# Kernel optimization log

Measured on AMD Instinct MI355X. Metric: run time of the kernel, lower is better.

Reference implementation:

```python
import jax, jax.numpy as jnp
import numpy as np

D = 256       # vec_dim
HEADS = 8     # head_num
PS = 4        # patch_size
WS = 7        # window_size (in patches)
P = WS * WS   # tokens per window


def _relative_index():
    # replicates the torch meshgrid / relative coord logic (indexing='ij')
    coords = np.stack(np.meshgrid(np.arange(WS), np.arange(WS), indexing='ij'))  # [2,WS,WS]
    cf = coords.reshape(2, -1)                                                   # [2,P]
    rc = (cf[:, :, None] - cf[:, None, :]).transpose(1, 2, 0)                    # [P,P,2]
    rc[:, :, 0] += WS - 1
    rc[:, :, 1] += WS - 1
    rc[:, :, 1] *= 2 * WS - 1
    return rc.sum(-1)  # [P,P] ints in [0,(2WS-1)^2)


def _shift_mask(ch, cw):
    # standard swin shift mask built on the patch grid (ch, cw)
    fm = np.zeros((ch, cw))
    idx = (slice(0, -WS), slice(-WS, -(WS // 2)), slice(-(WS // 2), None))
    cnt = 0
    for y in idx:
        for x in idx:
            fm[y, x] = cnt
            cnt += 1
    nh, nw = ch // WS, cw // WS
    fm = fm.reshape(nh, WS, nw, WS).transpose(0, 2, 1, 3).reshape(nh * nw, P)
    m = fm[:, None, :] - fm[:, :, None]
    return np.where(m != 0, -100.0, 0.0).astype(np.float32)


def setup_inputs() -> dict:
    key = jax.random.key(0)
    ks = jax.random.split(key, 10)
    N, PN = 8, 3136
    s = 0.02
    return {
        'inputs': jax.random.normal(ks[0], (N, D, PN), jnp.float32),
        'Wk': jax.random.normal(ks[1], (HEADS * D, D), jnp.float32) * s,
        'bk': jax.random.normal(ks[2], (HEADS * D,), jnp.float32) * s,
        'Wq': jax.random.normal(ks[3], (HEADS * D, D), jnp.float32) * s,
        'bq': jax.random.normal(ks[4], (HEADS * D,), jnp.float32) * s,
        'Wv': jax.random.normal(ks[5], (HEADS * D, D), jnp.float32) * s,
        'bv': jax.random.normal(ks[6], (HEADS * D,), jnp.float32) * s,
        'Wo': jax.random.normal(ks[7], (D, HEADS * D), jnp.float32) * s,
        'bo': jax.random.normal(ks[8], (D,), jnp.float32) * s,
        'rel_code': jax.random.normal(ks[9], ((2 * WS - 1) ** 2, HEADS), jnp.float32) * 0.02,
        'h': 224,
        'w': 224,
    }


def _forward(inputs, Wk, bk, Wq, bq, Wv, bv, Wo, bo, rel_code, h, w):
    ch, cw = h // PS, w // PS            # patch grid
    N, _, PN = inputs.shape
    C = D // (PS * PS)
    nh, nw = ch // WS, cw // WS
    WIN = nh * nw

    # patches2features -> pixel-space roll by WS//2 -> features2patches
    x = inputs.reshape(N, C, PS, PS, ch, cw)
    x = x.transpose(0, 1, 4, 2, 5, 3).reshape(N, C, ch * PS, cw * PS)
    x = jnp.roll(x, (WS // 2, WS // 2), axis=(-2, -1))
    x = x.reshape(N, C, ch, PS, cw, PS).transpose(0, 2, 4, 1, 3, 5).reshape(N, PN, D)
    x = x.transpose(0, 2, 1)  # [N,D,PN]

    def proj(W, b):
        e = jnp.einsum('od,ndp->nop', W, x) + b[None, :, None]  # [N,HEADS*D,PN]
        e = e.reshape(N, HEADS, D, ch, cw)
        # window partition: n h d (nh w1)(nw w2) -> n h (nh nw) d (w1 w2)
        e = e.reshape(N, HEADS, D, nh, WS, nw, WS)
        return e.transpose(0, 1, 3, 5, 2, 4, 6).reshape(N, HEADS, WIN, D, P)

    k = proj(Wk, bk)
    q = proj(Wq, bq)
    v = proj(Wv, bv)

    # attn[p,q] = k_p . q_q  (softmax over keys p, axis=3)
    attn = jnp.einsum('nhgdp,nhgdq->nhgpq', k, q) / (D ** 0.5)
    mask = jnp.asarray(_shift_mask(ch, cw))
    attn = attn + mask[None, None]
    rel_idx = _relative_index().ravel()
    rel = rel_code[rel_idx].reshape(P, P, HEADS).transpose(2, 0, 1)  # [H,P,P]
    attn = attn + rel[None, :, None]
    wmap = jax.nn.softmax(attn, axis=3)

    out = jnp.einsum('nhgdp,nhgpq->nhgdq', v, wmap)
    # window merge back to [N,H,D,PN]
    out = out.reshape(N, HEADS, nh, nw, D, WS, WS)
    out = out.transpose(0, 1, 4, 2, 5, 3, 6).reshape(N, HEADS * D, PN)
    return jnp.einsum('od,ndp->nop', Wo, out) + bo[None, :, None]  # [N,D,PN]


def reference(inputs, Wk, bk, Wq, bq, Wv, bv, Wo, bo, rel_code, h, w):
    return _forward(inputs, Wk, bk, Wq, bq, Wv, bv, Wo, bo, rel_code, h, w)
```

## Files before the change

### kernel.cpp

```cpp
#include <hip/hip_runtime.h>
#include <hip/hip_bf16.h>


#define NBATCH 8
#define TROWS  3200
#define FSTR   264

typedef unsigned short ushort_t;
typedef __attribute__((ext_vector_type(8))) short bf16x8;
typedef __attribute__((ext_vector_type(8))) unsigned short u16x8;
typedef __attribute__((ext_vector_type(4))) float f32x4;

__device__ __forceinline__ float b2f(ushort_t u) {
  union { unsigned int i; float f; } v; v.i = ((unsigned int)u) << 16; return v.f;
}
__device__ __forceinline__ ushort_t f2b(float f) {
  union { float f; unsigned int u; } v; v.f = f;
  unsigned int u = v.u;
  return (ushort_t)((u + 0x7FFFu + ((u >> 16) & 1u)) >> 16);
}
__device__ __forceinline__ int regof(int y) { return (y < 49) ? 0 : ((y < 53) ? 1 : 2); }
__device__ __forceinline__ int div7(int t) { return (t * 37) >> 8; }
__device__ __forceinline__ int tmap(int p, int gi, int gj) {
  int wi = div7(p); return (gi * 7 + wi) * 56 + gj * 7 + (p - wi * 7);
}
__device__ __forceinline__ ushort4 pack4(f32x4 a) {
  ushort4 u; u.x = f2b(a[0]); u.y = f2b(a[1]); u.z = f2b(a[2]); u.w = f2b(a[3]);
  return u;
}

__global__ void k_prep(const float* __restrict__ Wk, const float* __restrict__ Wq,
                       const float* __restrict__ Wo, const float* __restrict__ Wv,
                       const float* __restrict__ bk, const float* __restrict__ bq,
                       const float* __restrict__ bv, const float* __restrict__ bo,
                       const float* __restrict__ relc,
                       ushort_t* __restrict__ Aext, ushort_t* __restrict__ Wov3,
                       float* __restrict__ cvec, float* __restrict__ relL2) {
  __shared__ float red[8];
  int blk = blockIdx.x, t = threadIdx.x;
  if (blk < 512) {
    int h = blk >> 6, b0 = (blk & 63) << 2, a = t;
    const float* wkh = Wk + h * 65536;
    const float* wqh = Wq + h * 65536;
    float a0 = 0.f, a1 = 0.f, a2 = 0.f, a3 = 0.f;
    for (int dd = 0; dd < 256; ++dd) {
      float wk = wkh[dd * 256 + a];
      float4 w4 = *(const float4*)(wqh + dd * 256 + b0);
      a0 += wk * w4.x; a1 += wk * w4.y; a2 += wk * w4.z; a3 += wk * w4.w;
    }
    ushort4 u; u.x = f2b(a0); u.y = f2b(a1); u.z = f2b(a2); u.w = f2b(a3);
    *(ushort4*)(Aext + (h * 256 + a) * 256 + b0) = u;
  } else if (blk < 1024) {
    int bb = blk - 512;
    int h = bb >> 6, o0 = (bb & 63) << 2, d = t;
    float a0 = 0.f, a1 = 0.f, a2 = 0.f, a3 = 0.f;
    for (int dd = 0; dd < 256; ++dd) {
      float wv = Wv[(h * 256 + dd) * 256 + d];
      a0 += Wo[(o0 + 0) * 2048 + h * 256 + dd] * wv;
      a1 += Wo[(o0 + 1) * 2048 + h * 256 + dd] * wv;
      a2 += Wo[(o0 + 2) * 2048 + h * 256 + dd] * wv;
      a3 += Wo[(o0 + 3) * 2048 + h * 256 + dd] * wv;
    }
    Wov3[(o0 + 0) * 2048 + h * 256 + d] = f2b(a0);
    Wov3[(o0 + 1) * 2048 + h * 256 + d] = f2b(a1);
    Wov3[(o0 + 2) * 2048 + h * 256 + d] = f2b(a2);
    Wov3[(o0 + 3) * 2048 + h * 256 + d] = f2b(a3);
  } else if (blk < 1032) {
    int h = blk - 1024;
    float s1 = 0.f, s2 = 0.f;
    for (int dd = 0; dd < 256; ++dd) {
      s1 += bk[h * 256 + dd] * Wq[(h * 256 + dd) * 256 + t];
      s2 += bq[h * 256 + dd] * Wk[(h * 256 + dd) * 256 + t];
    }
    Aext[(2048 + h) * 256 + t] = f2b(s1);
    Aext[(2056 + h) * 256 + t] = f2b(s2);
  } else if (blk == 1032) {
    for (int i = t; i < 112 * 256 / 8; i += 256)
      *(u16x8*)(Aext + 2064 * 256 + i * 8) = (u16x8){0,0,0,0,0,0,0,0};
  } else if (blk < 1289) {
    int o = blk - 1033;
    const float* wob = Wo + o * 2048;
    float acc = 0.f;
#pragma unroll
    for (int j = 0; j < 8; ++j) acc += wob[j * 256 + t] * bv[j * 256 + t];
#pragma unroll
    for (int s = 1; s < 64; s <<= 1) acc += __shfl_xor(acc, s);
    if ((t & 63) == 0) red[t >> 6] = acc;
    __syncthreads();
    if (t == 0) cvec[o] = bo[o] + red[0] + red[1] + red[2] + red[3];
  } else {
    if (t < 8) {
      float c = 0.f;
      for (int dd = 0; dd < 256; ++dd) c += bk[t * 256 + dd] * bq[t * 256 + dd];
      red[t] = c * 0.0625f;
    }
    __syncthreads();
    for (int i = t; i < 8 * 169; i += 256) {
      int h = i / 169, idx = i - h * 169;
      relL2[i] = relc[idx * 8 + h] + red[h];
    }
  }
}

__global__ void k_conv(const float* __restrict__ X, ushort_t* __restrict__ Xroll) {
  const int n = blockIdx.x / 57, y = blockIdx.x % 57;
  ushort_t* xr = Xroll + (size_t)n * TROWS * 256;
  const int d = threadIdx.x;
  if (y == 56) {
    for (int i = d; i < 64 * 256 / 8; i += 256)
      *(u16x8*)(xr + 3136 * 256 + i * 8) = (u16x8){0,0,0,0,0,0,0,0};
    return;
  }
  const int c = d >> 4, p1 = (d >> 2) & 3, p2 = d & 3;
  const int sp = c * 16 + (((p1 + 1) & 3) << 2) + ((p2 + 1) & 3);
  const int ty = (p1 == 3) ? y : ((y == 0) ? 55 : y - 1);
  const float* rowp = X + (size_t)n * 256 * 3136 + sp * 3136 + ty * 56;
  ushort_t* orow = xr + y * 56 * 256 + d;
  for (int x = 0; x < 56; ++x) {
    int tx = (p2 == 3) ? x : ((x == 0) ? 55 : x - 1);
    orow[x * 256] = f2b(rowp[tx]);
  }
}

__global__ __launch_bounds__(512, 1) void k_fused(
    const ushort_t* __restrict__ Xroll, const ushort_t* __restrict__ Aext,
    const ushort_t* __restrict__ Wov3, const float* __restrict__ cvec,
    const float* __restrict__ relL2, float* __restrict__ out) {
  __shared__ ushort_t Xp[64 * FSTR];
  __shared__ ushort_t Msm[64 * FSTR];
  __shared__ ushort_t Tsm[64 * FSTR];
  __shared__ ushort_t StB[64 * 72];
  __shared__ float aqsL[8 * 64];
  __shared__ float bpsL[8 * 64];
  __shared__ float relLh[8 * 169];
  __shared__ float mPart[2][64];
  __shared__ float sPart[2][64];

  const int tid = threadIdx.x;
  const int wave = tid >> 6, lane = tid & 63;
  const int quad = lane >> 4, l16 = lane & 15;
  const int n = blockIdx.x & 7, g = blockIdx.x >> 3;
  const int gi = g >> 3, gj = g & 7;
  const ushort_t* Xn = Xroll + (size_t)n * TROWS * 256;
  float* on = out + (size_t)n * 256 * 3136;

  {
    const int p = tid & 63, cg = tid >> 6;
    if (p < 49) {
      int t = tmap(p, gi, gj);
#pragma unroll
      for (int i = 0; i < 4; ++i)
        *(u16x8*)(&Xp[p * FSTR + (cg * 4 + i) * 8]) =
            *(const u16x8*)(Xn + t * 256 + (cg * 4 + i) * 8);
    } else {
#pragma unroll
      for (int i = 0; i < 4; ++i)
        *(u16x8*)(&Xp[p * FSTR + (cg * 4 + i) * 8]) = (u16x8){0,0,0,0,0,0,0,0};
    }
  }
  for (int i = tid; i < 8 * 169; i += 512) relLh[i] = relL2[i];
  __syncthreads();

  const int wp = wave >> 2;
  const int wq = wave & 3;

  bf16x8 xb[8][2];
#pragma unroll
  for (int kk = 0; kk < 8; ++kk)
#pragma unroll
    for (int j = 0; j < 2; ++j)
      xb[kk][j] = *(const bf16x8*)(&Xp[((wp * 2 + j) * 16 + l16) * FSTR + kk * 32 + quad * 8]);

  bf16x8 xfr[2][2];
#pragma unroll
  for (int dt = 0; dt < 2; ++dt) {
    const int d = (wave * 2 + dt) * 16 + l16;
#pragma unroll
    for (int kk = 0; kk < 2; ++kk)
#pragma unroll
      for (int j = 0; j < 8; ++j)
        xfr[dt][kk][j] = (short)Xp[(kk * 32 + quad * 8 + j) * FSTR + d];
  }

  auto m_step = [&](int h) {
    f32x4 macc[2][4];
#pragma unroll
    for (int i = 0; i < 2; ++i)
#pragma unroll
      for (int t = 0; t < 4; ++t) macc[i][t] = (f32x4){0.f, 0.f, 0.f, 0.f};
    const ushort_t* Ah =
        Aext + (size_t)(h * 256 + wave * 32 + l16) * 256 + quad * 8;
#pragma unroll
    for (int kk = 0; kk < 8; ++kk) {
      bf16x8 ga[2];
#pragma unroll
      for (int i = 0; i < 2; ++i)
        ga[i] = *(const bf16x8*)(Ah + i * 16 * 256 + kk * 32);
#pragma unroll
      for (int t = 0; t < 4; ++t) {
        bf16x8 bx_ = *(const bf16x8*)(&Xp[(t * 16 + l16) * FSTR + kk * 32 + quad * 8]);
#pragma unroll
        for (int i = 0; i < 2; ++i)
          macc[i][t] = __builtin_amdgcn_mfma_f32_16x16x32_bf16(ga[i], bx_, macc[i][t], 0, 0, 0);
      }
    }
#pragma unroll
    for (int i = 0; i < 2; ++i)
#pragma unroll
      for (int t = 0; t < 4; ++t)
        *(ushort4*)(&Msm[(t * 16 + l16) * FSTR + wave * 32 + i * 16 + quad * 4]) =
            pack4(macc[i][t]);
  };

  m_step(0);
  if (wave == 0) {
    f32x4 eacc[4];
#pragma unroll
    for (int t = 0; t < 4; ++t) eacc[t] = (f32x4){0.f, 0.f, 0.f, 0.f};
    const ushort_t* Ae = Aext + (size_t)(2048 + l16) * 256 + quad * 8;
#pragma unroll
    for (int kk = 0; kk < 8; ++kk) {
      bf16x8 ea = *(const bf16x8*)(Ae + kk * 32);
#pragma unroll
      for (int t = 0; t < 4; ++t) {
        bf16x8 bx_ = *(const bf16x8*)(&Xp[(t * 16 + l16) * FSTR + kk * 32 + quad * 8]);
        eacc[t] = __builtin_amdgcn_mfma_f32_16x16x32_bf16(ea, bx_, eacc[t], 0, 0, 0);
      }
    }
#pragma unroll
    for (int t = 0; t < 4; ++t) {
      const int tok = t * 16 + l16;
#pragma unroll
      for (int r = 0; r < 4; ++r) {
        const int e = quad * 4 + r;
        if (e < 8) aqsL[e * 64 + tok] = eacc[t][r];
        else       bpsL[(e - 8) * 64 + tok] = eacc[t][r];
      }
    }
  }
  __syncthreads();

  const int q = wq * 16 + l16;
  const int qq = (q < 49) ? q : 48;
  const int yq = div7(qq), xq = qq - yq * 7;
  const int fq = regof(gi * 7 + yq) * 3 + regof(gj * 7 + xq);

  f32x4 oacc[2][4];
#pragma unroll
  for (int i = 0; i < 2; ++i)
#pragma unroll
    for (int j = 0; j < 4; ++j) oacc[i][j] = (f32x4){0.f, 0.f, 0.f, 0.f};

  for (int h = 0; h < 8; ++h) {
    f32x4 sa0[2], sa1[2];
    sa0[0] = (f32x4){0.f,0.f,0.f,0.f}; sa0[1] = (f32x4){0.f,0.f,0.f,0.f};
    sa1[0] = (f32x4){0.f,0.f,0.f,0.f}; sa1[1] = (f32x4){0.f,0.f,0.f,0.f};
#pragma unroll
    for (int kk = 0; kk < 8; kk += 2) {
      bf16x8 bfm0 = *(const bf16x8*)(&Msm[q * FSTR + kk * 32 + quad * 8]);
      bf16x8 bfm1 = *(const bf16x8*)(&Msm[q * FSTR + (kk + 1) * 32 + quad * 8]);
#pragma unroll
      for (int j = 0; j < 2; ++j) {
        sa0[j] = __builtin_amdgcn_mfma_f32_16x16x32_bf16(xb[kk][j], bfm0, sa0[j], 0, 0, 0);
        sa1[j] = __builtin_amdgcn_mfma_f32_16x16x32_bf16(xb[kk + 1][j], bfm1, sa1[j], 0, 0, 0);
      }
    }
    float v[8], ew[8];
    const float aqv = aqsL[h * 64 + q];
    const float* rel_h = &relLh[h * 169];
    float mw = -1e30f;
#pragma unroll
    for (int j = 0; j < 2; ++j)
#pragma unroll
      for (int r = 0; r < 4; ++r) {
        const int p = (wp * 2 + j) * 16 + quad * 4 + r;
        float val = -1e30f;
        if (p < 49) {
          const int yp = div7(p), xp = p - yp * 7;
          const int fp = regof(gi * 7 + yp) * 3 + regof(gj * 7 + xp);
          val = (sa0[j][r] + sa1[j][r] + aqv + bpsL[h * 64 + p]) * 0.0625f +
                rel_h[(yp - yq + 6) + 13 * (xp - xq + 6)];
          if (fp != fq) val -= 100.f;
        }
        v[j * 4 + r] = val;
        mw = fmaxf(mw, val);
      }
    mw = fmaxf(mw, __shfl_xor(mw, 16));
    mw = fmaxf(mw, __shfl_xor(mw, 32));
    float sw = 0.f;
#pragma unroll
    for (int i2 = 0; i2 < 8; ++i2) { ew[i2] = __expf(v[i2] - mw); sw += ew[i2]; }
    sw += __shfl_xor(sw, 16);
    sw += __shfl_xor(sw, 32);
    if (lane < 16) { mPart[wp][wq * 16 + lane] = mw; sPart[wp][wq * 16 + lane] = sw; }
    __syncthreads();
    {
      const float m0 = mPart[0][q], m1 = mPart[1][q];
      const float s0 = sPart[0][q], s1 = sPart[1][q];
      const float mg = fmaxf(m0, m1);
      const float tot = s0 * __expf(m0 - mg) + s1 * __expf(m1 - mg);
      const float scale = __expf(mw - mg) / tot;
#pragma unroll
      for (int j = 0; j < 2; ++j) {
        ushort4 u;
        u.x = f2b(ew[j * 4 + 0] * scale); u.y = f2b(ew[j * 4 + 1] * scale);
        u.z = f2b(ew[j * 4 + 2] * scale); u.w = f2b(ew[j * 4 + 3] * scale);
        *(ushort4*)(&StB[q * 72 + (wp * 2 + j) * 16 + quad * 4]) = u;
      }
    }
    if (h < 7) m_step(h + 1);
    __syncthreads();
    bf16x8 wfr[2][8];
#pragma unroll
    for (int i = 0; i < 2; ++i)
#pragma unroll
      for (int kk = 0; kk < 8; ++kk)
        wfr[i][kk] = *(const bf16x8*)(Wov3 +
            (size_t)(wave * 32 + i * 16 + l16) * 2048 + h * 256 + kk * 32 + quad * 8);
#pragma unroll
    for (int qt = 0; qt < 4; ++qt) {
      f32x4 tacc[2];
      tacc[0] = (f32x4){0.f, 0.f, 0.f, 0.f};
      tacc[1] = (f32x4){0.f, 0.f, 0.f, 0.f};
#pragma unroll
      for (int kk = 0; kk < 2; ++kk) {
        bf16x8 bfw = *(const bf16x8*)(&StB[(qt * 16 + l16) * 72 + kk * 32 + quad * 8]);
#pragma unroll
        for (int dt = 0; dt < 2; ++dt)
          tacc[dt] = __builtin_amdgcn_mfma_f32_16x16x32_bf16(xfr[dt][kk], bfw, tacc[dt], 0, 0, 0);
      }
#pragma unroll
      for (int dt = 0; dt < 2; ++dt)
        *(ushort4*)(&Tsm[(qt * 16 + l16) * FSTR + (wave * 2 + dt) * 16 + quad * 4]) =
            pack4(tacc[dt]);
    }
    __syncthreads();
#pragma unroll
    for (int kk = 0; kk < 8; ++kk) {
#pragma unroll
      for (int qt = 0; qt < 4; ++qt) {
        bf16x8 bfo = *(const bf16x8*)(&Tsm[(qt * 16 + l16) * FSTR + kk * 32 + quad * 8]);
#pragma unroll
        for (int i = 0; i < 2; ++i)
          oacc[i][qt] = __builtin_amdgcn_mfma_f32_16x16x32_bf16(wfr[i][kk], bfo, oacc[i][qt], 0, 0, 0);
      }
    }
  }
#pragma unroll
  for (int i = 0; i < 2; ++i) {
    const int ob = wave * 32 + i * 16 + quad * 4;
    const float4 cv = *(const float4*)(cvec + ob);
#pragma unroll
    for (int qt = 0; qt < 4; ++qt) {
      const int q2 = qt * 16 + l16;
      if (q2 < 49) {
        const int t2 = tmap(q2, gi, gj);
        on[(size_t)(ob + 0) * 3136 + t2] = oacc[i][qt][0] + cv.x;
        on[(size_t)(ob + 1) * 3136 + t2] = oacc[i][qt][1] + cv.y;
        on[(size_t)(ob + 2) * 3136 + t2] = oacc[i][qt][2] + cv.z;
        on[(size_t)(ob + 3) * 3136 + t2] = oacc[i][qt][3] + cv.w;
      }
    }
  }
}

extern "C" void kernel_launch(void* const* d_in, const int* in_sizes, int n_in,
                              void* d_out, int out_size, void* d_ws, size_t ws_size,
                              hipStream_t stream) {
  (void)in_sizes; (void)n_in; (void)out_size; (void)ws_size;
  const float* X  = (const float*)d_in[0];
  const float* Wk = (const float*)d_in[1];
  const float* bk = (const float*)d_in[2];
  const float* Wq = (const float*)d_in[3];
  const float* bq = (const float*)d_in[4];
  const float* Wv = (const float*)d_in[5];
  const float* bv = (const float*)d_in[6];
  const float* Wo = (const float*)d_in[7];
  const float* bo = (const float*)d_in[8];
  const float* rc = (const float*)d_in[9];

  ushort_t* Xroll = (ushort_t*)d_ws;
  ushort_t* Aext  = Xroll + (size_t)8 * TROWS * 256;
  ushort_t* Wov3  = Aext + 2176 * 256;
  float* fbase = (float*)(Wov3 + 256 * 2048);
  float* cvec  = fbase;
  float* relL2 = fbase + 256;
  float* out = (float*)d_out;

  k_prep <<<dim3(1290), dim3(256), 0, stream>>>(Wk, Wq, Wo, Wv, bk, bq, bv, bo, rc,
                                                Aext, Wov3, cvec, relL2);
  k_conv <<<dim3(8 * 57), dim3(256), 0, stream>>>(X, Xroll);
  k_fused<<<dim3(512), dim3(512), 0, stream>>>(Xroll, Aext, Wov3, cvec, relL2, out);
}
```

Before: 297.4 us.

## Double fused kernel block to 1024 threads and split per-wave work

The fused attention kernel now runs 16 waves per block instead of 8. Each wave's share of the M projection, score, softmax, T and output GEMMs is halved by re-partitioning tokens and output rows, and softmax partials are now combined across four wave groups. The Wo fragment loads are split into two halves to cut register pressure. The conv/roll kernel also loads each input row with vectorized float4 reads into registers instead of doing scalar gathered loads. The change aims for more latency hiding and fewer registers per wave, at the cost of more synchronization participants and a wider cross-wave softmax reduction.

```diff
diff --git a/kernel.cpp b/kernel.cpp
--- a/kernel.cpp
+++ b/kernel.cpp
@@ -116,13 +116,22 @@
   const int ty = (p1 == 3) ? y : ((y == 0) ? 55 : y - 1);
   const float* rowp = X + (size_t)n * 256 * 3136 + sp * 3136 + ty * 56;
   ushort_t* orow = xr + y * 56 * 256 + d;
+  float row[56];
+#pragma unroll
+  for (int i = 0; i < 14; ++i) {
+    const float4 t4 = ((const float4*)rowp)[i];
+    row[i * 4 + 0] = t4.x; row[i * 4 + 1] = t4.y;
+    row[i * 4 + 2] = t4.z; row[i * 4 + 3] = t4.w;
+  }
+  const bool nr = (p2 == 3);
+#pragma unroll
   for (int x = 0; x < 56; ++x) {
-    int tx = (p2 == 3) ? x : ((x == 0) ? 55 : x - 1);
-    orow[x * 256] = f2b(rowp[tx]);
-  }
-}
-
-__global__ __launch_bounds__(512, 1) void k_fused(
+    const float a = (x == 0) ? row[55] : row[x - 1];
+    orow[x * 256] = f2b(nr ? row[x] : a);
+  }
+}
+
+__global__ __launch_bounds__(1024, 4) void k_fused(
     const ushort_t* __restrict__ Xroll, const ushort_t* __restrict__ Aext,
     const ushort_t* __restrict__ Wov3, const float* __restrict__ cvec,
     const float* __restrict__ relL2, float* __restrict__ out) {
@@ -133,8 +142,8 @@
   __shared__ float aqsL[8 * 64];
   __shared__ float bpsL[8 * 64];
   __shared__ float relLh[8 * 169];
-  __shared__ float mPart[2][64];
-  __shared__ float sPart[2][64];
+  __shared__ float mPart[4][64];
+  __shared__ float sPart[4][64];
 
   const int tid = threadIdx.x;
   const int wave = tid >> 6, lane = tid & 63;
@@ -149,47 +158,47 @@
     if (p < 49) {
       int t = tmap(p, gi, gj);
 #pragma unroll
-      for (int i = 0; i < 4; ++i)
-        *(u16x8*)(&Xp[p * FSTR + (cg * 4 + i) * 8]) =
-            *(const u16x8*)(Xn + t * 256 + (cg * 4 + i) * 8);
+      for (int i = 0; i < 2; ++i)
+        *(u16x8*)(&Xp[p * FSTR + (cg * 2 + i) * 8]) =
+            *(const u16x8*)(Xn + t * 256 + (cg * 2 + i) * 8);
     } else {
 #pragma unroll
-      for (int i = 0; i < 4; ++i)
-        *(u16x8*)(&Xp[p * FSTR + (cg * 4 + i) * 8]) = (u16x8){0,0,0,0,0,0,0,0};
-    }
-  }
-  for (int i = tid; i < 8 * 169; i += 512) relLh[i] = relL2[i];
+      for (int i = 0; i < 2; ++i)
+        *(u16x8*)(&Xp[p * FSTR + (cg * 2 + i) * 8]) = (u16x8){0,0,0,0,0,0,0,0};
+    }
+  }
+  for (int i = tid; i < 8 * 169; i += 1024) relLh[i] = relL2[i];
   __syncthreads();
 
-  const int wp = wave >> 2;
-  const int wq = wave & 3;
-
-  bf16x8 xb[8][2];
+  const int wq  = wave & 3,  wpt = wave >> 2;
+  const int wb  = wave & 7,  th  = wave >> 3;
+  const int qp  = wave & 1,  dg  = wave >> 1;
+  const int wo  = wave & 7,  wq2 = wave >> 3;
+
+  bf16x8 xb[8];
 #pragma unroll
   for (int kk = 0; kk < 8; ++kk)
-#pragma unroll
-    for (int j = 0; j < 2; ++j)
-      xb[kk][j] = *(const bf16x8*)(&Xp[((wp * 2 + j) * 16 + l16) * FSTR + kk * 32 + quad * 8]);
+    xb[kk] = *(const bf16x8*)(&Xp[(wpt * 16 + l16) * FSTR + kk * 32 + quad * 8]);
 
   bf16x8 xfr[2][2];
 #pragma unroll
   for (int dt = 0; dt < 2; ++dt) {
-    const int d = (wave * 2 + dt) * 16 + l16;
+    const int dcol = (dg * 2 + dt) * 16 + l16;
 #pragma unroll
     for (int kk = 0; kk < 2; ++kk)
 #pragma unroll
       for (int j = 0; j < 8; ++j)
-        xfr[dt][kk][j] = (short)Xp[(kk * 32 + quad * 8 + j) * FSTR + d];
+        xfr[dt][kk][j] = (short)Xp[(kk * 32 + quad * 8 + j) * FSTR + dcol];
   }
 
   auto m_step = [&](int h) {
-    f32x4 macc[2][4];
+    f32x4 macc[2][2];
 #pragma unroll
     for (int i = 0; i < 2; ++i)
 #pragma unroll
-      for (int t = 0; t < 4; ++t) macc[i][t] = (f32x4){0.f, 0.f, 0.f, 0.f};
+      for (int t = 0; t < 2; ++t) macc[i][t] = (f32x4){0.f, 0.f, 0.f, 0.f};
     const ushort_t* Ah =
-        Aext + (size_t)(h * 256 + wave * 32 + l16) * 256 + quad * 8;
+        Aext + (size_t)(h * 256 + wb * 32 + l16) * 256 + quad * 8;
 #pragma unroll
     for (int kk = 0; kk < 8; ++kk) {
       bf16x8 ga[2];
@@ -197,8 +206,8 @@
       for (int i = 0; i < 2; ++i)
         ga[i] = *(const bf16x8*)(Ah + i * 16 * 256 + kk * 32);
 #pragma unroll
-      for (int t = 0; t < 4; ++t) {
-        bf16x8 bx_ = *(const bf16x8*)(&Xp[(t * 16 + l16) * FSTR + kk * 32 + quad * 8]);
+      for (int t = 0; t < 2; ++t) {
+        bf16x8 bx_ = *(const bf16x8*)(&Xp[(th * 32 + t * 16 + l16) * FSTR + kk * 32 + quad * 8]);
 #pragma unroll
         for (int i = 0; i < 2; ++i)
           macc[i][t] = __builtin_amdgcn_mfma_f32_16x16x32_bf16(ga[i], bx_, macc[i][t], 0, 0, 0);
@@ -207,8 +216,8 @@
 #pragma unroll
     for (int i = 0; i < 2; ++i)
 #pragma unroll
-      for (int t = 0; t < 4; ++t)
-        *(ushort4*)(&Msm[(t * 16 + l16) * FSTR + wave * 32 + i * 16 + quad * 4]) =
+      for (int t = 0; t < 2; ++t)
+        *(ushort4*)(&Msm[(th * 32 + t * 16 + l16) * FSTR + wb * 32 + i * 16 + quad * 4]) =
             pack4(macc[i][t]);
   };
 
@@ -245,114 +254,124 @@
   const int yq = div7(qq), xq = qq - yq * 7;
   const int fq = regof(gi * 7 + yq) * 3 + regof(gj * 7 + xq);
 
-  f32x4 oacc[2][4];
+  f32x4 oacc[2][2];
 #pragma unroll
   for (int i = 0; i < 2; ++i)
 #pragma unroll
-    for (int j = 0; j < 4; ++j) oacc[i][j] = (f32x4){0.f, 0.f, 0.f, 0.f};
+    for (int j = 0; j < 2; ++j) oacc[i][j] = (f32x4){0.f, 0.f, 0.f, 0.f};
 
   for (int h = 0; h < 8; ++h) {
-    f32x4 sa0[2], sa1[2];
-    sa0[0] = (f32x4){0.f,0.f,0.f,0.f}; sa0[1] = (f32x4){0.f,0.f,0.f,0.f};
-    sa1[0] = (f32x4){0.f,0.f,0.f,0.f}; sa1[1] = (f32x4){0.f,0.f,0.f,0.f};
+    f32x4 sa0 = (f32x4){0.f,0.f,0.f,0.f}, sa1 = (f32x4){0.f,0.f,0.f,0.f};
 #pragma unroll
     for (int kk = 0; kk < 8; kk += 2) {
       bf16x8 bfm0 = *(const bf16x8*)(&Msm[q * FSTR + kk * 32 + quad * 8]);
       bf16x8 bfm1 = *(const bf16x8*)(&Msm[q * FSTR + (kk + 1) * 32 + quad * 8]);
-#pragma unroll
-      for (int j = 0; j < 2; ++j) {
-        sa0[j] = __builtin_amdgcn_mfma_f32_16x16x32_bf16(xb[kk][j], bfm0, sa0[j], 0, 0, 0);
-        sa1[j] = __builtin_amdgcn_mfma_f32_16x16x32_bf16(xb[kk + 1][j], bfm1, sa1[j], 0, 0, 0);
-      }
-    }
-    float v[8], ew[8];
+      sa0 = __builtin_amdgcn_mfma_f32_16x16x32_bf16(xb[kk], bfm0, sa0, 0, 0, 0);
+      sa1 = __builtin_amdgcn_mfma_f32_16x16x32_bf16(xb[kk + 1], bfm1, sa1, 0, 0, 0);
+    }
+    float v[4], ew[4];
     const float aqv = aqsL[h * 64 + q];
     const float* rel_h = &relLh[h * 169];
     float mw = -1e30f;
 #pragma unroll
-    for (int j = 0; j < 2; ++j)
-#pragma unroll
-      for (int r = 0; r < 4; ++r) {
-        const int p = (wp * 2 + j) * 16 + quad * 4 + r;
-        float val = -1e30f;
-        if (p < 49) {
-          const int yp = div7(p), xp = p - yp * 7;
-          const int fp = regof(gi * 7 + yp) * 3 + regof(gj * 7 + xp);
-          val = (sa0[j][r] + sa1[j][r] + aqv + bpsL[h * 64 + p]) * 0.0625f +
-                rel_h[(yp - yq + 6) + 13 * (xp - xq + 6)];
-          if (fp != fq) val -= 100.f;
-        }
-        v[j * 4 + r] = val;
-        mw = fmaxf(mw, val);
-      }
+    for (int r = 0; r < 4; ++r) {
+      const int p = wpt * 16 + quad * 4 + r;
+      float val = -1e30f;
+      if (p < 49) {
+        const int yp = div7(p), xp = p - yp * 7;
+        const int fp = regof(gi * 7 + yp) * 3 + regof(gj * 7 + xp);
+        val = (sa0[r] + sa1[r] + aqv + bpsL[h * 64 + p]) * 0.0625f +
+              rel_h[(yp - yq + 6) + 13 * (xp - xq + 6)];
+        if (fp != fq) val -= 100.f;
+      }
+      v[r] = val;
+      mw = fmaxf(mw, val);
+    }
     mw = fmaxf(mw, __shfl_xor(mw, 16));
     mw = fmaxf(mw, __shfl_xor(mw, 32));
     float sw = 0.f;
 #pragma unroll
-    for (int i2 = 0; i2 < 8; ++i2) { ew[i2] = __expf(v[i2] - mw); sw += ew[i2]; }
+    for (int r = 0; r < 4; ++r) { ew[r] = __expf(v[r] - mw); sw += ew[r]; }
     sw += __shfl_xor(sw, 16);
     sw += __shfl_xor(sw, 32);
-    if (lane < 16) { mPart[wp][wq * 16 + lane] = mw; sPart[wp][wq * 16 + lane] = sw; }
+    if (lane < 16) { mPart[wpt][wq * 16 + lane] = mw; sPart[wpt][wq * 16 + lane] = sw; }
     __syncthreads();
     {
       const float m0 = mPart[0][q], m1 = mPart[1][q];
-      const float s0 = sPart[0][q], s1 = sPart[1][q];
-      const float mg = fmaxf(m0, m1);
-      const float tot = s0 * __expf(m0 - mg) + s1 * __expf(m1 - mg);
+      const float m2 = mPart[2][q], m3 = mPart[3][q];
+      const float mg = fmaxf(fmaxf(m0, m1), fmaxf(m2, m3));
+      const float tot = sPart[0][q] * __expf(m0 - mg) + sPart[1][q] * __expf(m1 - mg) +
+                        sPart[2][q] * __expf(m2 - mg) + sPart[3][q] * __expf(m3 - mg);
       const float scale = __expf(mw - mg) / tot;
-#pragma unroll
-      for (int j = 0; j < 2; ++j) {
-        ushort4 u;
-        u.x = f2b(ew[j * 4 + 0] * scale); u.y = f2b(ew[j * 4 + 1] * scale);
-        u.z = f2b(ew[j * 4 + 2] * scale); u.w = f2b(ew[j * 4 + 3] * scale);
-        *(ushort4*)(&StB[q * 72 + (wp * 2 + j) * 16 + quad * 4]) = u;
-      }
+      ushort4 u;
+      u.x = f2b(ew[0] * scale); u.y = f2b(ew[1] * scale);
+      u.z = f2b(ew[2] * scale); u.w = f2b(ew[3] * scale);
+      *(ushort4*)(&StB[q * 72 + wpt * 16 + quad * 4]) = u;
     }
     if (h < 7) m_step(h + 1);
     __syncthreads();
-    bf16x8 wfr[2][8];
+    const ushort_t* Wb = Wov3 + (size_t)(wo * 32 + l16) * 2048 + h * 256 + quad * 8;
+    bf16x8 wfrA[2][4];
 #pragma unroll
     for (int i = 0; i < 2; ++i)
 #pragma unroll
-      for (int kk = 0; kk < 8; ++kk)
-        wfr[i][kk] = *(const bf16x8*)(Wov3 +
-            (size_t)(wave * 32 + i * 16 + l16) * 2048 + h * 256 + kk * 32 + quad * 8);
-#pragma unroll
-    for (int qt = 0; qt < 4; ++qt) {
-      f32x4 tacc[2];
-      tacc[0] = (f32x4){0.f, 0.f, 0.f, 0.f};
-      tacc[1] = (f32x4){0.f, 0.f, 0.f, 0.f};
-#pragma unroll
-      for (int kk = 0; kk < 2; ++kk) {
-        bf16x8 bfw = *(const bf16x8*)(&StB[(qt * 16 + l16) * 72 + kk * 32 + quad * 8]);
+      for (int k = 0; k < 4; ++k)
+        wfrA[i][k] = *(const bf16x8*)(Wb + (size_t)i * 16 * 2048 + k * 32);
+    {
+      f32x4 tacc[2][2];
+#pragma unroll
+      for (int a = 0; a < 2; ++a)
+#pragma unroll
+        for (int b = 0; b < 2; ++b) tacc[a][b] = (f32x4){0.f, 0.f, 0.f, 0.f};
+#pragma unroll
+      for (int kk = 0; kk < 2; ++kk)
+#pragma unroll
+        for (int qt = 0; qt < 2; ++qt) {
+          bf16x8 bfw = *(const bf16x8*)(&StB[((qp * 2 + qt) * 16 + l16) * 72 + kk * 32 + quad * 8]);
+#pragma unroll
+          for (int dt = 0; dt < 2; ++dt)
+            tacc[qt][dt] = __builtin_amdgcn_mfma_f32_16x16x32_bf16(xfr[dt][kk], bfw, tacc[qt][dt], 0, 0, 0);
+        }
+#pragma unroll
+      for (int qt = 0; qt < 2; ++qt)
 #pragma unroll
         for (int dt = 0; dt < 2; ++dt)
-          tacc[dt] = __builtin_amdgcn_mfma_f32_16x16x32_bf16(xfr[dt][kk], bfw, tacc[dt], 0, 0, 0);
-      }
-#pragma unroll
-      for (int dt = 0; dt < 2; ++dt)
-        *(ushort4*)(&Tsm[(qt * 16 + l16) * FSTR + (wave * 2 + dt) * 16 + quad * 4]) =
-            pack4(tacc[dt]);
+          *(ushort4*)(&Tsm[((qp * 2 + qt) * 16 + l16) * FSTR + (dg * 2 + dt) * 16 + quad * 4]) =
+              pack4(tacc[qt][dt]);
     }
     __syncthreads();
 #pragma unroll
-    for (int kk = 0; kk < 8; ++kk) {
-#pragma unroll
-      for (int qt = 0; qt < 4; ++qt) {
-        bf16x8 bfo = *(const bf16x8*)(&Tsm[(qt * 16 + l16) * FSTR + kk * 32 + quad * 8]);
+    for (int k = 0; k < 4; ++k)
+#pragma unroll
+      for (int qt = 0; qt < 2; ++qt) {
+        bf16x8 bfo = *(const bf16x8*)(&Tsm[((wq2 * 2 + qt) * 16 + l16) * FSTR + k * 32 + quad * 8]);
 #pragma unroll
         for (int i = 0; i < 2; ++i)
-          oacc[i][qt] = __builtin_amdgcn_mfma_f32_16x16x32_bf16(wfr[i][kk], bfo, oacc[i][qt], 0, 0, 0);
-      }
-    }
+          oacc[i][qt] = __builtin_amdgcn_mfma_f32_16x16x32_bf16(wfrA[i][k], bfo, oacc[i][qt], 0, 0, 0);
+      }
+    bf16x8 wfrB[2][4];
+#pragma unroll
+    for (int i = 0; i < 2; ++i)
+#pragma unroll
+      for (int k = 0; k < 4; ++k)
+        wfrB[i][k] = *(const bf16x8*)(Wb + (size_t)i * 16 * 2048 + (4 + k) * 32);
+#pragma unroll
+    for (int k = 0; k < 4; ++k)
+#pragma unroll
+      for (int qt = 0; qt < 2; ++qt) {
+        bf16x8 bfo = *(const bf16x8*)(&Tsm[((wq2 * 2 + qt) * 16 + l16) * FSTR + (4 + k) * 32 + quad * 8]);
+#pragma unroll
+        for (int i = 0; i < 2; ++i)
+          oacc[i][qt] = __builtin_amdgcn_mfma_f32_16x16x32_bf16(wfrB[i][k], bfo, oacc[i][qt], 0, 0, 0);
+      }
   }
 #pragma unroll
   for (int i = 0; i < 2; ++i) {
-    const int ob = wave * 32 + i * 16 + quad * 4;
+    const int ob = wo * 32 + i * 16 + quad * 4;
     const float4 cv = *(const float4*)(cvec + ob);
 #pragma unroll
-    for (int qt = 0; qt < 4; ++qt) {
-      const int q2 = qt * 16 + l16;
+    for (int qt = 0; qt < 2; ++qt) {
+      const int q2 = (wq2 * 2 + qt) * 16 + l16;
       if (q2 < 49) {
         const int t2 = tmap(q2, gi, gj);
         on[(size_t)(ob + 0) * 3136 + t2] = oacc[i][qt][0] + cv.x;
@@ -390,5 +409,5 @@
   k_prep <<<dim3(1290), dim3(256), 0, stream>>>(Wk, Wq, Wo, Wv, bk, bq, bv, bo, rc,
                                                 Aext, Wov3, cvec, relL2);
   k_conv <<<dim3(8 * 57), dim3(256), 0, stream>>>(X, Xroll);
-  k_fused<<<dim3(512), dim3(512), 0, stream>>>(Xroll, Aext, Wov3, cvec, relL2, out);
-}
+  k_fused<<<dim3(512), dim3(1024), 0, stream>>>(Xroll, Aext, Wov3, cvec, relL2, out);
+}
```

Result: slower. 434.9 us (+46.2%).
